# Optimization experiments

Measured on AMD Instinct MI355X. Metric: run time of the kernel, lower is better.

Reference implementation:

```python
import jax, jax.numpy as jnp
import numpy as np

DECAY = 0.99
EPS = 1e-05


def setup_inputs() -> dict:
    key = jax.random.key(0)
    k1, k2, k3 = jax.random.split(key, 3)
    inp = jax.random.normal(k1, (8, 1024, 512), dtype=jnp.float32)
    embed = jax.random.normal(k2, (512, 8192), dtype=jnp.float32)
    # buffers: cluster_size starts at zeros, embed_avg is a clone of embed in torch
    cluster_size = jnp.zeros((8192,), dtype=jnp.float32)
    embed_avg = embed
    return {"input": inp, "embed": embed, "cluster_size": cluster_size, "embed_avg": embed_avg}


def reference(input, embed, cluster_size, embed_avg):
    dim, n_embed = embed.shape
    flatten = input.reshape(-1, dim)  # [N, dim]
    # squared euclidean distance via expansion: ||f||^2 - 2 f.E + ||E||^2 -> [N, n_embed]
    dist = ((flatten ** 2).sum(axis=1, keepdims=True)
            - 2.0 * flatten @ embed
            + (embed ** 2).sum(axis=0, keepdims=True))
    embed_ind_flat = jnp.argmin(dist, axis=1)  # argmax of -dist == argmin of dist
    embed_ind = embed_ind_flat.reshape(input.shape[:-1])
    # nearest-codebook lookup: F.embedding(ind, embed.T)
    quantize = jnp.take(embed.T, embed_ind, axis=0)  # [..., dim]
    # training-mode EMA statistics (one-hot scatter sums, done without a dense one-hot)
    onehot_sum = jnp.zeros((n_embed,), flatten.dtype).at[embed_ind_flat].add(1.0)
    embed_sum = jax.ops.segment_sum(flatten, embed_ind_flat, num_segments=n_embed).T  # [dim, n_embed]
    new_cluster_size = cluster_size * DECAY + (1.0 - DECAY) * onehot_sum
    new_embed_avg = embed_avg * DECAY + (1.0 - DECAY) * embed_sum
    n = new_cluster_size.sum()
    cs = (new_cluster_size + EPS) / (n + n_embed * EPS) * n
    new_embed = new_embed_avg / cs[None, :]
    # commitment loss (quantize detached) and straight-through estimator
    diff = jnp.mean((jax.lax.stop_gradient(quantize) - input) ** 2)
    quantize_st = input + jax.lax.stop_gradient(quantize - input)
    return (quantize_st, diff, embed_ind, new_embed, new_cluster_size, new_embed_avg)
```

## Files before the change

kernel.cpp:

```cpp
#include <hip/hip_runtime.h>


constexpr int N = 8192;
constexpr int K = 512;
constexpr int M = 8192;

typedef unsigned short ushortT;
typedef __attribute__((ext_vector_type(8))) short s8v;
typedef __attribute__((ext_vector_type(4))) float f4v;

__device__ __forceinline__ ushortT f2bf(float x) {
    unsigned u = __float_as_uint(x);
    unsigned r = (u + 0x7FFFu + ((u >> 16) & 1u)) >> 16;
    return (ushortT)r;
}
__device__ __forceinline__ float bf2f(ushortT h) {
    return __uint_as_float(((unsigned)h) << 16);
}

typedef const __attribute__((address_space(1))) unsigned gau;
typedef __attribute__((address_space(3))) unsigned lau;
__device__ __forceinline__ void gl16(const void* g, void* l) {
    __builtin_amdgcn_global_load_lds((gau*)g, (lau*)l, 16, 0, 0);
}

__device__ __forceinline__ unsigned packDI(float d, int col) {
    unsigned u = __float_as_uint(d);
    unsigned s = (u & 0x80000000u) ? ~u : (u | 0x80000000u);
    return (s & ~0x1FFFu) | (unsigned)col;
}
__device__ __forceinline__ float unpackD(unsigned p) {
    unsigned s = p & ~0x1FFFu;
    unsigned u = (s & 0x80000000u) ? (s & 0x7fffffffu) : ~s;
    return __uint_as_float(u);
}
__device__ __forceinline__ void top2u(unsigned& a, unsigned& b, unsigned c) {
    unsigned mn = c < a ? c : a;
    unsigned mx = c < a ? a : c;
    a = mn;
    b = mx < b ? mx : b;
}

__global__ __launch_bounds__(256) void k_prep(
    const float* __restrict__ f, const float* __restrict__ E,
    ushortT* __restrict__ Fh, ushortT* __restrict__ EhT, ushortT* __restrict__ ElT,
    float* __restrict__ c, float* __restrict__ counts) {
    __shared__ float tile[64][65];
    int b = blockIdx.x, t = threadIdx.x;
    if (b < 2048) {
        size_t i8 = ((size_t)b * 256 + t) * 8;
        float4 x0 = *(const float4*)&f[i8];
        float4 x1 = *(const float4*)&f[i8 + 4];
        float xs[8] = {x0.x, x0.y, x0.z, x0.w, x1.x, x1.y, x1.z, x1.w};
        union { s8v v; ushortT u[8]; } h;
#pragma unroll
        for (int j = 0; j < 8; ++j) h.u[j] = f2bf(xs[j]);
        *(s8v*)&Fh[i8] = h.v;
    } else if (b < 3072) {
        int bb = b - 2048;
        int jb = bb & 127, kb = bb >> 7;
        int jj = t & 63, kk0 = t >> 6;
        int j0 = jb * 64, k0 = kb * 64;
#pragma unroll
        for (int it = 0; it < 16; ++it) {
            int kk = it * 4 + kk0;
            tile[kk][jj] = E[(size_t)(k0 + kk) * M + j0 + jj];
        }
        __syncthreads();
        int r = t >> 2, ks = (t & 3) * 16;
        union { s8v v[2]; ushortT u[16]; } h, lo;
#pragma unroll
        for (int i = 0; i < 16; ++i) {
            float x = tile[ks + i][r];
            ushortT hh = f2bf(x);
            h.u[i] = hh;
            lo.u[i] = f2bf(x - bf2f(hh));
        }
        size_t o = (size_t)(j0 + r) * K + k0 + ks;
        *(s8v*)&EhT[o] = h.v[0];
        *(s8v*)&EhT[o + 8] = h.v[1];
        *(s8v*)&ElT[o] = lo.v[0];
        *(s8v*)&ElT[o + 8] = lo.v[1];
    } else {
        int j = (b - 3072) * 256 + t;
        float s = 0.f;
#pragma unroll 8
        for (int k = 0; k < K; ++k) {
            float e = E[(size_t)k * M + j];
            s = fmaf(e, e, s);
        }
        c[j] = s;
        counts[j] = 0.f;
    }
}

__global__ __launch_bounds__(512) void k_score(
    const ushortT* __restrict__ Fh, const ushortT* __restrict__ Eh,
    const float* __restrict__ cE, unsigned* __restrict__ pv) {
    __shared__ alignas(16) ushortT ls[2][2][256 * 64];

    int bid = blockIdx.x;
    int xcd = bid & 7, local = bid >> 3;
    int rb = xcd * 4 + (local & 3);
    int cb = local >> 2;
    int rowBase = rb * 256, colBase = cb * 256;
    int tid = threadIdx.x;
    int w = tid >> 6, l = tid & 63;
    int wr = w >> 2, wc = w & 3;
    int l15 = l & 15, g4 = l >> 4;
    int s7 = l15 & 7;

    const ushortT* srcA = Fh + (size_t)(rowBase + w * 32) * K;
    const ushortT* srcB = Eh + (size_t)(colBase + w * 32) * K;

    f4v acc[8][4];
#pragma unroll
    for (int m = 0; m < 8; ++m)
#pragma unroll
        for (int n = 0; n < 4; ++n) acc[m][n] = (f4v){0.f, 0.f, 0.f, 0.f};

#define STAGE(p, ch)                                                  \
    do {                                                              \
        _Pragma("unroll")                                             \
        for (int i_ = 0; i_ < 4; ++i_) {                              \
            int q_ = i_ * 64 + l;                                     \
            int row_ = q_ >> 3, slot_ = q_ & 7;                       \
            int swz_ = (slot_ ^ (row_ & 7)) * 8;                      \
            size_t so_ = (size_t)row_ * K + (ch) * 64 + swz_;         \
            gl16(srcA + so_, &ls[p][0][w * 2048 + q_ * 8]);           \
            gl16(srcB + so_, &ls[p][1][w * 2048 + q_ * 8]);           \
        }                                                             \
    } while (0)

    STAGE(0, 0);
    __syncthreads();

    for (int ch = 0; ch < 8; ++ch) {
        int p = ch & 1;
        if (ch < 7) STAGE(p ^ 1, ch + 1);
#pragma unroll
        for (int kk = 0; kk < 2; ++kk) {
            s8v a[8], b[4];
#pragma unroll
            for (int m = 0; m < 8; ++m) {
                int rA = wr * 128 + m * 16 + l15;
                a[m] = *(const s8v*)&ls[p][0][rA * 64 + ((kk * 4 + g4) ^ s7) * 8];
            }
#pragma unroll
            for (int n = 0; n < 4; ++n) {
                int rB = wc * 64 + n * 16 + l15;
                b[n] = *(const s8v*)&ls[p][1][rB * 64 + ((kk * 4 + g4) ^ s7) * 8];
            }
#pragma unroll
            for (int m = 0; m < 8; ++m)
#pragma unroll
                for (int n = 0; n < 4; ++n)
                    acc[m][n] = __builtin_amdgcn_mfma_f32_16x16x32_bf16(
                        a[m], b[n], acc[m][n], 0, 0, 0);
        }
        __syncthreads();
    }
#undef STAGE

    float cj[4];
#pragma unroll
    for (int n = 0; n < 4; ++n) cj[n] = cE[colBase + wc * 64 + n * 16 + l15];
    unsigned* cand = (unsigned*)ls;

#pragma unroll
    for (int m = 0; m < 8; ++m)
#pragma unroll
        for (int q = 0; q < 4; ++q) {
            unsigned p0 = packDI(fmaf(-2.f, acc[m][0][q], cj[0]), colBase + wc * 64 + l15);
            unsigned p1 = packDI(fmaf(-2.f, acc[m][1][q], cj[1]), colBase + wc * 64 + 16 + l15);
            unsigned p2 = packDI(fmaf(-2.f, acc[m][2][q], cj[2]), colBase + wc * 64 + 32 + l15);
            unsigned p3 = packDI(fmaf(-2.f, acc[m][3][q], cj[3]), colBase + wc * 64 + 48 + l15);
            unsigned a_ = p0 < p1 ? p0 : p1;
            unsigned b_ = p0 < p1 ? p1 : p0;
            top2u(a_, b_, p2);
            top2u(a_, b_, p3);
#pragma unroll
            for (int mk = 8; mk >= 2; mk >>= 1) {
                unsigned oa = __shfl_xor((int)a_, mk);
                unsigned ob = __shfl_xor((int)b_, mk);
                top2u(a_, b_, oa);
                top2u(a_, b_, ob);
            }
            if (l15 < 2) {
                int row = wr * 128 + m * 16 + g4 * 4 + q;
                int slot = wc * 4 + l15 * 2;
                cand[row * 17 + slot] = a_;
                cand[row * 17 + slot + 1] = b_;
            }
        }
    __syncthreads();
    if (tid < 256) {
        unsigned best = cand[tid * 17], second = cand[tid * 17 + 1];
#pragma unroll
        for (int i = 2; i < 16; i += 2) {
            top2u(best, second, cand[tid * 17 + i]);
            top2u(best, second, cand[tid * 17 + i + 1]);
        }
        size_t o = (size_t)(rowBase + tid) * 64 + cb * 2;
        pv[o] = best;
        pv[o + 1] = second;
    }
}

__global__ __launch_bounds__(256) void k_combine(
    const unsigned* __restrict__ pv, const float* __restrict__ f,
    const ushortT* __restrict__ EhT, const ushortT* __restrict__ ElT,
    const float* __restrict__ cE,
    int* __restrict__ indws, float* __restrict__ o_ind, float* __restrict__ counts,
    float* __restrict__ o_q, float* __restrict__ diffp) {
    __shared__ float dsum[4];
    int w = threadIdx.x >> 6, l = threadIdx.x & 63;
    int row = blockIdx.x * 4 + w;
    unsigned e = pv[(size_t)row * 64 + l];
    unsigned mn = e;
#pragma unroll
    for (int m = 1; m < 64; m <<= 1) {
        unsigned o = __shfl_xor((int)mn, m);
        mn = o < mn ? o : mn;
    }
    float thr = unpackD(mn) + 2.0f;
    float dl = unpackD(e);
    float bestd = 3.4e38f; int bestj = 0x7fffffff;
    float4 fa = *(const float4*)&f[(size_t)row * K + l * 8];
    float4 fb = *(const float4*)&f[(size_t)row * K + l * 8 + 4];
    float fx[8] = {fa.x, fa.y, fa.z, fa.w, fb.x, fb.y, fb.z, fb.w};
    s8v qh, ql;
    unsigned long long mask = __ballot(dl <= thr);
    while (mask) {
        int b = __ffsll(mask) - 1;
        mask &= mask - 1;
        int j = (int)(__shfl((int)e, b) & 0x1fff);
        s8v hv = *(const s8v*)(EhT + (size_t)j * K + l * 8);
        s8v lv = *(const s8v*)(ElT + (size_t)j * K + l * 8);
        float a = 0.f;
#pragma unroll
        for (int q = 0; q < 8; ++q)
            a = fmaf(fx[q], bf2f((ushortT)hv[q]) + bf2f((ushortT)lv[q]), a);
#pragma unroll
        for (int m = 1; m < 64; m <<= 1) a += __shfl_xor(a, m);
        float d = cE[j] - 2.f * a;
        if (d < bestd || (d == bestd && j < bestj)) {
            bestd = d; bestj = j; qh = hv; ql = lv;
        }
    }
    float os[8];
    float local = 0.f;
#pragma unroll
    for (int q = 0; q < 8; ++q) {
        float qv = bf2f((ushortT)qh[q]) + bf2f((ushortT)ql[q]);
        float d = qv - fx[q];
        os[q] = fx[q] + d;
        local = fmaf(d, d, local);
    }
    float4 o0 = {os[0], os[1], os[2], os[3]};
    float4 o1 = {os[4], os[5], os[6], os[7]};
    *(float4*)&o_q[(size_t)row * K + l * 8] = o0;
    *(float4*)&o_q[(size_t)row * K + l * 8 + 4] = o1;
#pragma unroll
    for (int m = 1; m < 64; m <<= 1) local += __shfl_xor(local, m);
    if (l == 0) {
        indws[row] = bestj;
        o_ind[row] = (float)bestj;
        atomicAdd(&counts[bestj], 1.0f);
        dsum[w] = local;
    }
    __syncthreads();
    if (threadIdx.x == 0)
        diffp[blockIdx.x] = dsum[0] + dsum[1] + dsum[2] + dsum[3];
}

__global__ __launch_bounds__(256) void k_ema(
    const float* __restrict__ f, const int* __restrict__ indws,
    const float* __restrict__ ea, float* __restrict__ o_avg,
    const float* __restrict__ cs_in, const float* __restrict__ counts,
    float* __restrict__ o_ncs, float* __restrict__ csr,
    const float* __restrict__ diffp, float* __restrict__ o_diff) {
    int b = blockIdx.x, t = threadIdx.x;
    if (b == 256) {
        __shared__ float wsum[4];
        __shared__ float nsh;
        float myncs[32];
        float loc = 0.f;
#pragma unroll 32
        for (int i = 0; i < 32; ++i) {
            int j = i * 256 + t;
            float v = 0.99f * cs_in[j] + 0.01f * counts[j];
            myncs[i] = v;
            o_ncs[j] = v;
            loc += v;
        }
#pragma unroll
        for (int off = 32; off; off >>= 1) loc += __shfl_down(loc, off);
        if ((t & 63) == 0) wsum[t >> 6] = loc;
        __syncthreads();
        if (t == 0) nsh = wsum[0] + wsum[1] + wsum[2] + wsum[3];
        __syncthreads();
        float n = nsh;
#pragma unroll 32
        for (int i = 0; i < 32; ++i) {
            int j = i * 256 + t;
            csr[j] = (myncs[i] + 1e-5f) / (n + 8192.0f * 1e-5f) * n;
        }
        float dl = 0.f;
#pragma unroll
        for (int i = 0; i < 8; ++i) dl += diffp[i * 256 + t];
#pragma unroll
        for (int off = 32; off; off >>= 1) dl += __shfl_down(dl, off);
        __syncthreads();
        if ((t & 63) == 0) wsum[t >> 6] = dl;
        __syncthreads();
        if (t == 0)
            o_diff[0] = (wsum[0] + wsum[1] + wsum[2] + wsum[3]) * (1.0f / 4194304.0f);
        return;
    }
    __shared__ float acc[512 * 33];
    __shared__ int q[8192];
    __shared__ int qn;
    for (int i = t; i < 512 * 33; i += 256) acc[i] = 0.f;
    if (t == 0) qn = 0;
    __syncthreads();
    for (int r = t; r < N; r += 256) {
        int j = indws[r];
        if ((j >> 5) == b) {
            int s = atomicAdd(&qn, 1);
            q[s] = (r << 5) | (j & 31);
        }
    }
    __syncthreads();
    int nq = qn;
    int s = 0;
    for (; s + 4 <= nq; s += 4) {
        int e0 = q[s], e1 = q[s + 1], e2 = q[s + 2], e3 = q[s + 3];
        float a0 = f[(size_t)(e0 >> 5) * K + t],       c0 = f[(size_t)(e0 >> 5) * K + t + 256];
        float a1 = f[(size_t)(e1 >> 5) * K + t],       c1 = f[(size_t)(e1 >> 5) * K + t + 256];
        float a2 = f[(size_t)(e2 >> 5) * K + t],       c2 = f[(size_t)(e2 >> 5) * K + t + 256];
        float a3 = f[(size_t)(e3 >> 5) * K + t],       c3 = f[(size_t)(e3 >> 5) * K + t + 256];
        acc[t * 33 + (e0 & 31)] += a0;         acc[(t + 256) * 33 + (e0 & 31)] += c0;
        acc[t * 33 + (e1 & 31)] += a1;         acc[(t + 256) * 33 + (e1 & 31)] += c1;
        acc[t * 33 + (e2 & 31)] += a2;         acc[(t + 256) * 33 + (e2 & 31)] += c2;
        acc[t * 33 + (e3 & 31)] += a3;         acc[(t + 256) * 33 + (e3 & 31)] += c3;
    }
    for (; s < nq; ++s) {
        int e = q[s];
        float a0 = f[(size_t)(e >> 5) * K + t];
        float c0 = f[(size_t)(e >> 5) * K + t + 256];
        acc[t * 33 + (e & 31)] += a0;
        acc[(t + 256) * 33 + (e & 31)] += c0;
    }
    __syncthreads();
    for (int i = t; i < 512 * 32; i += 256) {
        int d = i >> 5, c = i & 31;
        size_t o = (size_t)d * M + b * 32 + c;
        o_avg[o] = 0.99f * ea[o] + 0.01f * acc[d * 33 + c];
    }
}

__global__ void k_div(const float* __restrict__ avg, const float* __restrict__ csr,
                      float* __restrict__ o_ne) {
    size_t idx = (size_t)blockIdx.x * 256 + threadIdx.x;
    size_t el = idx * 4;
    float4 a = *(const float4*)&avg[el];
    int j = (int)(el & (size_t)(M - 1));
    float4 cc = *(const float4*)&csr[j];
    float4 r;
    r.x = a.x / cc.x; r.y = a.y / cc.y; r.z = a.z / cc.z; r.w = a.w / cc.w;
    *(float4*)&o_ne[el] = r;
}

extern "C" void kernel_launch(void* const* d_in, const int* in_sizes, int n_in,
                              void* d_out, int out_size, void* d_ws, size_t ws_size,
                              hipStream_t stream) {
    const float* f     = (const float*)d_in[0];
    const float* E     = (const float*)d_in[1];
    const float* cs_in = (const float*)d_in[2];
    const float* ea    = (const float*)d_in[3];

    float* out = (float*)d_out;
    float* o_q    = out;
    float* o_diff = out + 4194304;
    float* o_ind  = out + 4194305;
    float* o_ne   = out + 4202497;
    float* o_ncs  = out + 8396801;
    float* o_avg  = out + 8404993;

    ushortT* Fh  = (ushortT*)o_q;
    ushortT* EhT = (ushortT*)o_ne;
    ushortT* ElT = EhT + (size_t)M * K;
    unsigned* pv = (unsigned*)o_avg;

    float* wsf    = (float*)d_ws;
    float* c      = wsf;
    float* counts = wsf + 8192;
    float* csr    = wsf + 16384;
    int*   indws  = (int*)(wsf + 24576);
    float* diffp  = wsf + 32768;

    k_prep   <<<3104, 256, 0, stream>>>(f, E, Fh, EhT, ElT, c, counts);
    k_score  <<<1024, 512, 0, stream>>>(Fh, EhT, c, pv);
    k_combine<<<2048, 256, 0, stream>>>(pv, f, EhT, ElT, c, indws, o_ind, counts,
                                        o_q, diffp);
    k_ema    <<<257, 256, 0, stream>>>(f, indws, ea, o_avg,
                                       cs_in, counts, o_ncs, csr,
                                       diffp, o_diff);
    k_div    <<<4096, 256, 0, stream>>>(o_avg, csr, o_ne);
}
```

Baseline: 181.3 us.

## Fuse codebook norms into transpose pass and fold division into EMA kernel

Codebook squared norms are now produced as per-64-row partial sums during the bf16 transpose tile pass, which replaces the separate 32-block strided column-reduction path. k_score and k_combine each sum the 8 partials when they need a norm. The final divide kernel is removed: each EMA block recomputes the total cluster count itself and writes new_embed alongside new_embed_avg, saving a full read and write of the 16MB matrix. The cost is redundant reduction work in all 256 EMA blocks and extra partial loads in the scorer. The main chunk loop in the scorer is also fully unrolled.

New measurement: 161.0 us. -11.2%, faster.

```diff
diff --git a/kernel.cpp b/kernel.cpp
--- a/kernel.cpp
+++ b/kernel.cpp
@@ -44,10 +44,11 @@
 __global__ __launch_bounds__(256) void k_prep(
     const float* __restrict__ f, const float* __restrict__ E,
     ushortT* __restrict__ Fh, ushortT* __restrict__ EhT, ushortT* __restrict__ ElT,
-    float* __restrict__ c, float* __restrict__ counts) {
+    float* __restrict__ pc, float* __restrict__ counts) {
     __shared__ float tile[64][65];
     int b = blockIdx.x, t = threadIdx.x;
     if (b < 2048) {
+        if (b < 32) counts[b * 256 + t] = 0.f;
         size_t i8 = ((size_t)b * 256 + t) * 8;
         float4 x0 = *(const float4*)&f[i8];
         float4 x1 = *(const float4*)&f[i8 + 4];
@@ -56,7 +57,7 @@
 #pragma unroll
         for (int j = 0; j < 8; ++j) h.u[j] = f2bf(xs[j]);
         *(s8v*)&Fh[i8] = h.v;
-    } else if (b < 3072) {
+    } else {
         int bb = b - 2048;
         int jb = bb & 127, kb = bb >> 7;
         int jj = t & 63, kk0 = t >> 6;
@@ -69,9 +70,11 @@
         __syncthreads();
         int r = t >> 2, ks = (t & 3) * 16;
         union { s8v v[2]; ushortT u[16]; } h, lo;
+        float nrm = 0.f;
 #pragma unroll
         for (int i = 0; i < 16; ++i) {
             float x = tile[ks + i][r];
+            nrm = fmaf(x, x, nrm);
             ushortT hh = f2bf(x);
             h.u[i] = hh;
             lo.u[i] = f2bf(x - bf2f(hh));
@@ -81,22 +84,15 @@
         *(s8v*)&EhT[o + 8] = h.v[1];
         *(s8v*)&ElT[o] = lo.v[0];
         *(s8v*)&ElT[o + 8] = lo.v[1];
-    } else {
-        int j = (b - 3072) * 256 + t;
-        float s = 0.f;
-#pragma unroll 8
-        for (int k = 0; k < K; ++k) {
-            float e = E[(size_t)k * M + j];
-            s = fmaf(e, e, s);
-        }
-        c[j] = s;
-        counts[j] = 0.f;
+        nrm += __shfl_down(nrm, 2);
+        nrm += __shfl_down(nrm, 1);
+        if ((t & 3) == 0) pc[(size_t)kb * M + j0 + r] = nrm;
     }
 }
 
 __global__ __launch_bounds__(512) void k_score(
     const ushortT* __restrict__ Fh, const ushortT* __restrict__ Eh,
-    const float* __restrict__ cE, unsigned* __restrict__ pv) {
+    const float* __restrict__ pc, unsigned* __restrict__ pv) {
     __shared__ alignas(16) ushortT ls[2][2][256 * 64];
 
     int bid = blockIdx.x;
@@ -135,6 +131,7 @@
     STAGE(0, 0);
     __syncthreads();
 
+#pragma unroll
     for (int ch = 0; ch < 8; ++ch) {
         int p = ch & 1;
         if (ch < 7) STAGE(p ^ 1, ch + 1);
@@ -164,7 +161,13 @@
 
     float cj[4];
 #pragma unroll
-    for (int n = 0; n < 4; ++n) cj[n] = cE[colBase + wc * 64 + n * 16 + l15];
+    for (int n = 0; n < 4; ++n) {
+        int col = colBase + wc * 64 + n * 16 + l15;
+        float s = 0.f;
+#pragma unroll
+        for (int kb = 0; kb < 8; ++kb) s += pc[(size_t)kb * M + col];
+        cj[n] = s;
+    }
     unsigned* cand = (unsigned*)ls;
 
 #pragma unroll
@@ -210,7 +213,7 @@
 __global__ __launch_bounds__(256) void k_combine(
     const unsigned* __restrict__ pv, const float* __restrict__ f,
     const ushortT* __restrict__ EhT, const ushortT* __restrict__ ElT,
-    const float* __restrict__ cE,
+    const float* __restrict__ pc,
     int* __restrict__ indws, float* __restrict__ o_ind, float* __restrict__ counts,
     float* __restrict__ o_q, float* __restrict__ diffp) {
     __shared__ float dsum[4];
@@ -243,7 +246,10 @@
             a = fmaf(fx[q], bf2f((ushortT)hv[q]) + bf2f((ushortT)lv[q]), a);
 #pragma unroll
         for (int m = 1; m < 64; m <<= 1) a += __shfl_xor(a, m);
-        float d = cE[j] - 2.f * a;
+        float cj = 0.f;
+#pragma unroll
+        for (int kb = 0; kb < 8; ++kb) cj += pc[(size_t)kb * M + j];
+        float d = cj - 2.f * a;
         if (d < bestd || (d == bestd && j < bestj)) {
             bestd = d; bestj = j; qh = hv; ql = lv;
         }
@@ -276,51 +282,36 @@
 
 __global__ __launch_bounds__(256) void k_ema(
     const float* __restrict__ f, const int* __restrict__ indws,
-    const float* __restrict__ ea, float* __restrict__ o_avg,
+    const float* __restrict__ ea, float* __restrict__ o_avg, float* __restrict__ o_ne,
     const float* __restrict__ cs_in, const float* __restrict__ counts,
-    float* __restrict__ o_ncs, float* __restrict__ csr,
+    float* __restrict__ o_ncs,
     const float* __restrict__ diffp, float* __restrict__ o_diff) {
     int b = blockIdx.x, t = threadIdx.x;
+    __shared__ float wsum[4];
     if (b == 256) {
-        __shared__ float wsum[4];
-        __shared__ float nsh;
-        float myncs[32];
         float loc = 0.f;
 #pragma unroll 32
         for (int i = 0; i < 32; ++i) {
             int j = i * 256 + t;
-            float v = 0.99f * cs_in[j] + 0.01f * counts[j];
-            myncs[i] = v;
-            o_ncs[j] = v;
-            loc += v;
-        }
-#pragma unroll
-        for (int off = 32; off; off >>= 1) loc += __shfl_down(loc, off);
-        if ((t & 63) == 0) wsum[t >> 6] = loc;
-        __syncthreads();
-        if (t == 0) nsh = wsum[0] + wsum[1] + wsum[2] + wsum[3];
-        __syncthreads();
-        float n = nsh;
-#pragma unroll 32
-        for (int i = 0; i < 32; ++i) {
-            int j = i * 256 + t;
-            csr[j] = (myncs[i] + 1e-5f) / (n + 8192.0f * 1e-5f) * n;
+            o_ncs[j] = 0.99f * cs_in[j] + 0.01f * counts[j];
         }
         float dl = 0.f;
 #pragma unroll
         for (int i = 0; i < 8; ++i) dl += diffp[i * 256 + t];
 #pragma unroll
         for (int off = 32; off; off >>= 1) dl += __shfl_down(dl, off);
-        __syncthreads();
         if ((t & 63) == 0) wsum[t >> 6] = dl;
         __syncthreads();
         if (t == 0)
             o_diff[0] = (wsum[0] + wsum[1] + wsum[2] + wsum[3]) * (1.0f / 4194304.0f);
+        (void)loc;
         return;
     }
     __shared__ float acc[512 * 33];
     __shared__ int q[8192];
     __shared__ int qn;
+    __shared__ float csr_s[32];
+    __shared__ float nsh;
     for (int i = t; i < 512 * 33; i += 256) acc[i] = 0.f;
     if (t == 0) qn = 0;
     __syncthreads();
@@ -352,24 +343,33 @@
         acc[t * 33 + (e & 31)] += a0;
         acc[(t + 256) * 33 + (e & 31)] += c0;
     }
+    float loc = 0.f;
+#pragma unroll 32
+    for (int i = 0; i < 32; ++i) {
+        int j = i * 256 + t;
+        loc += 0.99f * cs_in[j] + 0.01f * counts[j];
+    }
+#pragma unroll
+    for (int off = 32; off; off >>= 1) loc += __shfl_down(loc, off);
+    __syncthreads();
+    if ((t & 63) == 0) wsum[t >> 6] = loc;
+    __syncthreads();
+    if (t == 0) nsh = wsum[0] + wsum[1] + wsum[2] + wsum[3];
+    __syncthreads();
+    if (t < 32) {
+        int j = b * 32 + t;
+        float v = 0.99f * cs_in[j] + 0.01f * counts[j];
+        float n = nsh;
+        csr_s[t] = (v + 1e-5f) / (n + 8192.0f * 1e-5f) * n;
+    }
     __syncthreads();
     for (int i = t; i < 512 * 32; i += 256) {
         int d = i >> 5, c = i & 31;
         size_t o = (size_t)d * M + b * 32 + c;
-        o_avg[o] = 0.99f * ea[o] + 0.01f * acc[d * 33 + c];
-    }
-}
-
-__global__ void k_div(const float* __restrict__ avg, const float* __restrict__ csr,
-                      float* __restrict__ o_ne) {
-    size_t idx = (size_t)blockIdx.x * 256 + threadIdx.x;
-    size_t el = idx * 4;
-    float4 a = *(const float4*)&avg[el];
-    int j = (int)(el & (size_t)(M - 1));
-    float4 cc = *(const float4*)&csr[j];
-    float4 r;
-    r.x = a.x / cc.x; r.y = a.y / cc.y; r.z = a.z / cc.z; r.w = a.w / cc.w;
-    *(float4*)&o_ne[el] = r;
+        float val = 0.99f * ea[o] + 0.01f * acc[d * 33 + c];
+        o_avg[o] = val;
+        o_ne[o] = val / csr_s[c];
+    }
 }
 
 extern "C" void kernel_launch(void* const* d_in, const int* in_sizes, int n_in,
@@ -394,18 +394,16 @@
     unsigned* pv = (unsigned*)o_avg;
 
     float* wsf    = (float*)d_ws;
-    float* c      = wsf;
     float* counts = wsf + 8192;
-    float* csr    = wsf + 16384;
     int*   indws  = (int*)(wsf + 24576);
     float* diffp  = wsf + 32768;
-
-    k_prep   <<<3104, 256, 0, stream>>>(f, E, Fh, EhT, ElT, c, counts);
-    k_score  <<<1024, 512, 0, stream>>>(Fh, EhT, c, pv);
-    k_combine<<<2048, 256, 0, stream>>>(pv, f, EhT, ElT, c, indws, o_ind, counts,
+    float* pc     = wsf + 40960;
+
+    k_prep   <<<3072, 256, 0, stream>>>(f, E, Fh, EhT, ElT, pc, counts);
+    k_score  <<<1024, 512, 0, stream>>>(Fh, EhT, pc, pv);
+    k_combine<<<2048, 256, 0, stream>>>(pv, f, EhT, ElT, pc, indws, o_ind, counts,
                                         o_q, diffp);
-    k_ema    <<<257, 256, 0, stream>>>(f, indws, ea, o_avg,
-                                       cs_in, counts, o_ncs, csr,
+    k_ema    <<<257, 256, 0, stream>>>(f, indws, ea, o_avg, o_ne,
+                                       cs_in, counts, o_ncs,
                                        diffp, o_diff);
-    k_div    <<<4096, 256, 0, stream>>>(o_avg, csr, o_ne);
-}
+}
```
